# Performance work log

Measured on AMD Instinct MI355X. Metric: run time of the kernel, lower is better.

## Reference

```python
import jax, jax.numpy as jnp
import numpy as np

NEG_SLOPE = 0.2

def setup_inputs() -> dict:
    key = jax.random.key(0)
    ks = jax.random.split(key, 6)
    N, C, H, E_DIM, E = 50000, 128, 64, 16, 800000
    x = jax.random.normal(ks[0], (N, C), dtype=jnp.float32)
    edge_index = jax.random.randint(ks[1], (2, E), 0, N, dtype=jnp.int64)
    edge_attr = jax.random.normal(ks[2], (E, E_DIM), dtype=jnp.float32)
    fc_w = jax.random.normal(ks[3], (H, C), dtype=jnp.float32) * (1.0 / np.sqrt(C))
    fc_b = jnp.zeros((H,), dtype=jnp.float32)
    att_w = jax.random.normal(ks[4], (H, 2 * H + E_DIM), dtype=jnp.float32) * (1.0 / np.sqrt(2 * H + E_DIM))
    att_b = jnp.zeros((H,), dtype=jnp.float32)
    return {"x": x, "edge_index": edge_index, "edge_attr": edge_attr,
            "fc_w": fc_w, "fc_b": fc_b, "att_w": att_w, "att_b": att_b}

def reference(x, edge_index, edge_attr, fc_w, fc_b, att_w, att_b):
    # Node projection: h = fc(x), [N, H]
    h = x @ fc_w.T + fc_b
    src = edge_index[0]  # i (destination of aggregation)
    dst = edge_index[1]  # j (neighbor whose features are aggregated)
    h_i = h[src]                      # [E, H]
    h_j = h[dst]                      # [E, H]
    feat = jnp.concatenate([h_i, h_j, edge_attr], axis=-1)  # [E, 2H+edge_dim]
    alpha = jax.nn.leaky_relu(feat @ att_w.T + att_b, negative_slope=NEG_SLOPE)  # [E, H]
    # dropout is identity in eval mode (training=False)
    msg = h_j * alpha                 # [E, H]
    out = jax.ops.segment_sum(msg, src, num_segments=h.shape[0])  # scatter-add into out[i]
    return out
```

## Files before the change

kernel.cpp:

```cpp
#include <hip/hip_runtime.h>


__global__ __launch_bounds__(256) void node_kernel(
    const float* __restrict__ x,
    const float* __restrict__ fc_w, const float* __restrict__ fc_b,
    const float* __restrict__ att_w, const float* __restrict__ att_b,
    float* __restrict__ ai_out, float2* __restrict__ hjaj_out, int N)
{
    __shared__ __align__(16) float4 wF[64 * 32];
    __shared__ __align__(16) float4 wI[64 * 16];
    __shared__ __align__(16) float4 wJ[64 * 16];
    __shared__ __align__(16) float xs[4][4][128];
    __shared__ __align__(16) float hs[4][4][64];

    const int t = threadIdx.x;
    for (int idx = t; idx < 64 * 32; idx += 256) {
        int l = idx >> 5, c = idx & 31;
        wF[l * 32 + (c ^ (l & 31))] =
            *reinterpret_cast<const float4*>(fc_w + l * 128 + c * 4);
    }
    for (int idx = t; idx < 64 * 16; idx += 256) {
        int l = idx >> 4, c = idx & 15;
        wI[l * 16 + (c ^ (l & 15))] =
            *reinterpret_cast<const float4*>(att_w + l * 144 + c * 4);
        wJ[l * 16 + (c ^ (l & 15))] =
            *reinterpret_cast<const float4*>(att_w + l * 144 + 64 + c * 4);
    }
    __syncthreads();

    const int w = t >> 6, l = t & 63;
    const float bF = fc_b[l];
    const float bA = att_b[l];
    const int waveId = blockIdx.x * 4 + w;
    const int nWaves = gridDim.x * 4;
    const float2* x2 = reinterpret_cast<const float2*>(x);

    for (int n0 = waveId * 4; n0 < N; n0 += nWaves * 4) {
        const int nb = min(4, N - n0);
        #pragma unroll
        for (int m = 0; m < 4; ++m) {
            if (m < nb) {
                float2 xv = x2[(size_t)(n0 + m) * 64 + l];
                xs[w][m][2 * l] = xv.x;
                xs[w][m][2 * l + 1] = xv.y;
            }
        }
        float acc[4] = {bF, bF, bF, bF};
        #pragma unroll
        for (int c = 0; c < 32; ++c) {
            float4 wv = wF[l * 32 + (c ^ (l & 31))];
            #pragma unroll
            for (int m = 0; m < 4; ++m) {
                float4 xc = *reinterpret_cast<const float4*>(&xs[w][m][c * 4]);
                acc[m] = fmaf(wv.x, xc.x, acc[m]);
                acc[m] = fmaf(wv.y, xc.y, acc[m]);
                acc[m] = fmaf(wv.z, xc.z, acc[m]);
                acc[m] = fmaf(wv.w, xc.w, acc[m]);
            }
        }
        #pragma unroll
        for (int m = 0; m < 4; ++m) hs[w][m][l] = acc[m];
        float a2[4] = {bA, bA, bA, bA};
        float a3[4] = {0.f, 0.f, 0.f, 0.f};
        #pragma unroll
        for (int c = 0; c < 16; ++c) {
            float4 wi = wI[l * 16 + (c ^ (l & 15))];
            float4 wj = wJ[l * 16 + (c ^ (l & 15))];
            #pragma unroll
            for (int m = 0; m < 4; ++m) {
                float4 hv = *reinterpret_cast<const float4*>(&hs[w][m][c * 4]);
                a2[m] = fmaf(wi.x, hv.x, a2[m]); a2[m] = fmaf(wi.y, hv.y, a2[m]);
                a2[m] = fmaf(wi.z, hv.z, a2[m]); a2[m] = fmaf(wi.w, hv.w, a2[m]);
                a3[m] = fmaf(wj.x, hv.x, a3[m]); a3[m] = fmaf(wj.y, hv.y, a3[m]);
                a3[m] = fmaf(wj.z, hv.z, a3[m]); a3[m] = fmaf(wj.w, hv.w, a3[m]);
            }
        }
        #pragma unroll
        for (int m = 0; m < 4; ++m) {
            if (m < nb) {
                ai_out[(size_t)(n0 + m) * 64 + l] = a2[m];
                hjaj_out[(size_t)(n0 + m) * 64 + l] = make_float2(acc[m], a3[m]);
            }
        }
    }
}

__global__ __launch_bounds__(256) void edge_kernel(
    const int* __restrict__ ei,
    const float* __restrict__ ea,
    const float* __restrict__ ai,
    const float2* __restrict__ hjaj,
    const float* __restrict__ att_w,
    float* __restrict__ out, int E)
{
    __shared__ __align__(16) float4 eas[4][256];

    const int t = threadIdx.x;
    const int w = t >> 6, l = t & 63;

    float we[16];
    #pragma unroll
    for (int k = 0; k < 16; ++k) we[k] = att_w[l * 144 + 128 + k];

    const int waveId = blockIdx.x * 4 + w;
    const int nWaves = gridDim.x * 4;
    const float4* ea4 = reinterpret_cast<const float4*>(ea);
    const int fullE = E & ~63;

#define EDGE_COMPUTE(S, HD, IDX)                                               \
    {                                                                          \
        float4 v0 = eas[w][(IDX) * 4 + 0];                                     \
        float4 v1 = eas[w][(IDX) * 4 + 1];                                     \
        float4 v2 = eas[w][(IDX) * 4 + 2];                                     \
        float4 v3 = eas[w][(IDX) * 4 + 3];                                     \
        float pre = (HD).y + a_##S;                                            \
        pre = fmaf(we[0], v0.x, pre);  pre = fmaf(we[1], v0.y, pre);           \
        pre = fmaf(we[2], v0.z, pre);  pre = fmaf(we[3], v0.w, pre);           \
        pre = fmaf(we[4], v1.x, pre);  pre = fmaf(we[5], v1.y, pre);           \
        pre = fmaf(we[6], v1.z, pre);  pre = fmaf(we[7], v1.w, pre);           \
        pre = fmaf(we[8], v2.x, pre);  pre = fmaf(we[9], v2.y, pre);           \
        pre = fmaf(we[10], v2.z, pre); pre = fmaf(we[11], v2.w, pre);          \
        pre = fmaf(we[12], v3.x, pre); pre = fmaf(we[13], v3.y, pre);          \
        pre = fmaf(we[14], v3.z, pre); pre = fmaf(we[15], v3.w, pre);          \
        float alpha = pre > 0.f ? pre : 0.2f * pre;                            \
        atomicAdd(&out[(size_t)s_##S * 64 + l], (HD).x * alpha);               \
    }

    for (int e0 = waveId * 64; e0 < fullE; e0 += nWaves * 64) {
        int src = ei[e0 + l];
        int dst = ei[E + e0 + l];
        #pragma unroll
        for (int r = 0; r < 4; ++r)
            eas[w][r * 64 + l] = ea4[(size_t)e0 * 4 + r * 64 + l];
        asm volatile("s_waitcnt lgkmcnt(0)" ::: "memory");

        #pragma unroll 1
        for (int g = 0; g < 64; g += 4) {
            int s_0 = __shfl(src, g + 0), s_1 = __shfl(src, g + 1);
            int s_2 = __shfl(src, g + 2), s_3 = __shfl(src, g + 3);
            int d_0 = __shfl(dst, g + 0), d_1 = __shfl(dst, g + 1);
            int d_2 = __shfl(dst, g + 2), d_3 = __shfl(dst, g + 3);
            float a_0 = ai[(size_t)s_0 * 64 + l];
            float a_1 = ai[(size_t)s_1 * 64 + l];
            float a_2 = ai[(size_t)s_2 * 64 + l];
            float a_3 = ai[(size_t)s_3 * 64 + l];
            float2 h0 = hjaj[(size_t)d_0 * 64 + l];
            float2 h1 = hjaj[(size_t)d_1 * 64 + l];
            float2 h2 = hjaj[(size_t)d_2 * 64 + l];
            float2 h3 = hjaj[(size_t)d_3 * 64 + l];
            EDGE_COMPUTE(0, h0, g + 0);
            EDGE_COMPUTE(1, h1, g + 1);
            EDGE_COMPUTE(2, h2, g + 2);
            EDGE_COMPUTE(3, h3, g + 3);
        }
    }

    if (E > fullE && waveId == 0) {
        const int nE = E - fullE;
        int src = 0, dst = 0;
        if (l < nE) { src = ei[fullE + l]; dst = ei[E + fullE + l]; }
        #pragma unroll
        for (int r = 0; r < 4; ++r) {
            int f = r * 64 + l;
            if (f < nE * 4) eas[w][f] = ea4[(size_t)fullE * 4 + f];
        }
        asm volatile("s_waitcnt lgkmcnt(0)" ::: "memory");
        for (int e = 0; e < nE; ++e) {
            int s_0 = __shfl(src, e);
            int d_0 = __shfl(dst, e);
            float a_0 = ai[(size_t)s_0 * 64 + l];
            float2 h0 = hjaj[(size_t)d_0 * 64 + l];
            EDGE_COMPUTE(0, h0, e);
        }
    }
#undef EDGE_COMPUTE
}

extern "C" void kernel_launch(void* const* d_in, const int* in_sizes, int n_in,
                              void* d_out, int out_size, void* d_ws, size_t ws_size,
                              hipStream_t stream) {
    const float* x     = (const float*)d_in[0];
    const int*   ei    = (const int*)d_in[1];
    const float* ea    = (const float*)d_in[2];
    const float* fc_w  = (const float*)d_in[3];
    const float* fc_b  = (const float*)d_in[4];
    const float* att_w = (const float*)d_in[5];
    const float* att_b = (const float*)d_in[6];
    float* out = (float*)d_out;

    const int N = in_sizes[0] / 128;
    const int E = in_sizes[2] / 16;

    float*  ai   = (float*)d_ws;
    float2* hjaj = (float2*)((char*)d_ws + (size_t)N * 64 * sizeof(float));

    hipMemsetAsync(d_out, 0, (size_t)out_size * sizeof(float), stream);

    node_kernel<<<512, 256, 0, stream>>>(x, fc_w, fc_b, att_w, att_b, ai, hjaj, N);
    edge_kernel<<<2048, 256, 0, stream>>>(ei, ea, ai, hjaj, att_w, out, E);
}
```

Before: 266.8 us.

## Pipeline edge gathers via async global-to-LDS loads with double buffering

Restructures the edge kernel so each wave handles exactly one 64-edge tile and gathers the per-node rows (ai, h, aj) straight into LDS using global_load_lds. Loads are issued in 8-edge chunks into two alternating buffers, with explicit vmcnt waits so gathers overlap compute and atomics. The interleaved h/aj float2 layout is split into separate arrays so each gather is a 4-byte-per-lane load into LDS. The grid grows to one wave per tile with 128-thread blocks, and the hand-tuned vmcnt counts depend on exact instruction ordering, which is fragile.

```diff
diff --git a/kernel.cpp b/kernel.cpp
--- a/kernel.cpp
+++ b/kernel.cpp
@@ -1,11 +1,25 @@
 #include <hip/hip_runtime.h>
 
 
-__global__ __launch_bounds__(256) void node_kernel(
+#define GLDS4(gp, lp)                                                          \
+    __builtin_amdgcn_global_load_lds(                                          \
+        (const __attribute__((address_space(1))) unsigned int*)(gp),           \
+        (__attribute__((address_space(3))) unsigned int*)(lp), 4, 0, 0)
+#define GLDS16(gp, lp)                                                         \
+    __builtin_amdgcn_global_load_lds(                                          \
+        (const __attribute__((address_space(1))) unsigned int*)(gp),           \
+        (__attribute__((address_space(3))) unsigned int*)(lp), 16, 0, 0)
+
+#define WAITVM_(n) asm volatile("s_waitcnt vmcnt(" #n ")" ::: "memory")
+#define WAITVM(n)                                                              \
+    do { WAITVM_(n); __builtin_amdgcn_sched_barrier(0); } while (0)
+
+__global__ __launch_bounds__(256, 2) void node_kernel(
     const float* __restrict__ x,
     const float* __restrict__ fc_w, const float* __restrict__ fc_b,
     const float* __restrict__ att_w, const float* __restrict__ att_b,
-    float* __restrict__ ai_out, float2* __restrict__ hjaj_out, int N)
+    float* __restrict__ ai_out, float* __restrict__ h_out,
+    float* __restrict__ aj_out, int N)
 {
     __shared__ __align__(16) float4 wF[64 * 32];
     __shared__ __align__(16) float4 wI[64 * 16];
@@ -79,101 +93,128 @@
         for (int m = 0; m < 4; ++m) {
             if (m < nb) {
                 ai_out[(size_t)(n0 + m) * 64 + l] = a2[m];
-                hjaj_out[(size_t)(n0 + m) * 64 + l] = make_float2(acc[m], a3[m]);
+                h_out[(size_t)(n0 + m) * 64 + l]  = acc[m];
+                aj_out[(size_t)(n0 + m) * 64 + l] = a3[m];
             }
         }
     }
 }
 
-__global__ __launch_bounds__(256) void edge_kernel(
+__global__ __launch_bounds__(128) void edge_kernel(
     const int* __restrict__ ei,
     const float* __restrict__ ea,
     const float* __restrict__ ai,
-    const float2* __restrict__ hjaj,
+    const float* __restrict__ hv,
+    const float* __restrict__ aj,
     const float* __restrict__ att_w,
     float* __restrict__ out, int E)
 {
-    __shared__ __align__(16) float4 eas[4][256];
-
-    const int t = threadIdx.x;
-    const int w = t >> 6, l = t & 63;
+    __shared__ __align__(16) float lds[2][4096];
+
+    const int t = threadIdx.x, w = t >> 6, l = t & 63;
+    float* L = lds[w];
+    float* ea_s = L;
+    float* bufA = L + 1024;
+    float* bufB = L + 2560;
 
     float we[16];
     #pragma unroll
     for (int k = 0; k < 16; ++k) we[k] = att_w[l * 144 + 128 + k];
 
-    const int waveId = blockIdx.x * 4 + w;
-    const int nWaves = gridDim.x * 4;
-    const float4* ea4 = reinterpret_cast<const float4*>(ea);
-    const int fullE = E & ~63;
-
-#define EDGE_COMPUTE(S, HD, IDX)                                               \
+    const int waveId = blockIdx.x * 2 + w;
+    const int e0 = waveId * 64;
+    if (e0 >= E) return;
+    const int nE = min(64, E - e0);
+
+    int src = 0, dst = 0;
+    if (l < nE) { src = ei[e0 + l]; dst = ei[E + e0 + l]; }
+
+#define ISSUE(c, buf)                                                          \
     {                                                                          \
-        float4 v0 = eas[w][(IDX) * 4 + 0];                                     \
-        float4 v1 = eas[w][(IDX) * 4 + 1];                                     \
-        float4 v2 = eas[w][(IDX) * 4 + 2];                                     \
-        float4 v3 = eas[w][(IDX) * 4 + 3];                                     \
-        float pre = (HD).y + a_##S;                                            \
-        pre = fmaf(we[0], v0.x, pre);  pre = fmaf(we[1], v0.y, pre);           \
-        pre = fmaf(we[2], v0.z, pre);  pre = fmaf(we[3], v0.w, pre);           \
-        pre = fmaf(we[4], v1.x, pre);  pre = fmaf(we[5], v1.y, pre);           \
-        pre = fmaf(we[6], v1.z, pre);  pre = fmaf(we[7], v1.w, pre);           \
-        pre = fmaf(we[8], v2.x, pre);  pre = fmaf(we[9], v2.y, pre);           \
-        pre = fmaf(we[10], v2.z, pre); pre = fmaf(we[11], v2.w, pre);          \
-        pre = fmaf(we[12], v3.x, pre); pre = fmaf(we[13], v3.y, pre);          \
-        pre = fmaf(we[14], v3.z, pre); pre = fmaf(we[15], v3.w, pre);          \
-        float alpha = pre > 0.f ? pre : 0.2f * pre;                            \
-        atomicAdd(&out[(size_t)s_##S * 64 + l], (HD).x * alpha);               \
-    }
-
-    for (int e0 = waveId * 64; e0 < fullE; e0 += nWaves * 64) {
-        int src = ei[e0 + l];
-        int dst = ei[E + e0 + l];
+        _Pragma("unroll") for (int k = 0; k < 8; ++k) {                        \
+            int e_ = (c) * 8 + k;                                              \
+            int s_ = __shfl(src, e_);                                          \
+            int d_ = __shfl(dst, e_);                                          \
+            GLDS4(ai + (size_t)s_ * 64 + l, (buf) + k * 192);                  \
+            GLDS4(hv + (size_t)d_ * 64 + l, (buf) + k * 192 + 64);             \
+            GLDS4(aj + (size_t)d_ * 64 + l, (buf) + k * 192 + 128);            \
+        }                                                                      \
+    }
+
+#define FMA16(pre, v0, v1, v2, v3)                                             \
+    pre = fmaf(we[0], (v0).x, pre);  pre = fmaf(we[1], (v0).y, pre);           \
+    pre = fmaf(we[2], (v0).z, pre);  pre = fmaf(we[3], (v0).w, pre);           \
+    pre = fmaf(we[4], (v1).x, pre);  pre = fmaf(we[5], (v1).y, pre);           \
+    pre = fmaf(we[6], (v1).z, pre);  pre = fmaf(we[7], (v1).w, pre);           \
+    pre = fmaf(we[8], (v2).x, pre);  pre = fmaf(we[9], (v2).y, pre);           \
+    pre = fmaf(we[10], (v2).z, pre); pre = fmaf(we[11], (v2).w, pre);          \
+    pre = fmaf(we[12], (v3).x, pre); pre = fmaf(we[13], (v3).y, pre);          \
+    pre = fmaf(we[14], (v3).z, pre); pre = fmaf(we[15], (v3).w, pre)
+
+#define COMPUTE(c, buf)                                                        \
+    {                                                                          \
+        _Pragma("unroll") for (int k = 0; k < 8; ++k) {                        \
+            int e_ = (c) * 8 + k;                                              \
+            int s_ = __shfl(src, e_);                                          \
+            float av = (buf)[k * 192 + l];                                     \
+            float hh = (buf)[k * 192 + 64 + l];                                \
+            float a2 = (buf)[k * 192 + 128 + l];                               \
+            const float4* eav = reinterpret_cast<const float4*>(ea_s + e_ * 16); \
+            float4 v0 = eav[0], v1 = eav[1], v2 = eav[2], v3 = eav[3];         \
+            float pre = av + a2;                                               \
+            FMA16(pre, v0, v1, v2, v3);                                        \
+            float alpha = pre > 0.f ? pre : 0.2f * pre;                        \
+            atomicAdd(&out[(size_t)s_ * 64 + l], hh * alpha);                  \
+        }                                                                      \
+    }
+
+    if (nE == 64) {
         #pragma unroll
         for (int r = 0; r < 4; ++r)
-            eas[w][r * 64 + l] = ea4[(size_t)e0 * 4 + r * 64 + l];
-        asm volatile("s_waitcnt lgkmcnt(0)" ::: "memory");
-
-        #pragma unroll 1
-        for (int g = 0; g < 64; g += 4) {
-            int s_0 = __shfl(src, g + 0), s_1 = __shfl(src, g + 1);
-            int s_2 = __shfl(src, g + 2), s_3 = __shfl(src, g + 3);
-            int d_0 = __shfl(dst, g + 0), d_1 = __shfl(dst, g + 1);
-            int d_2 = __shfl(dst, g + 2), d_3 = __shfl(dst, g + 3);
-            float a_0 = ai[(size_t)s_0 * 64 + l];
-            float a_1 = ai[(size_t)s_1 * 64 + l];
-            float a_2 = ai[(size_t)s_2 * 64 + l];
-            float a_3 = ai[(size_t)s_3 * 64 + l];
-            float2 h0 = hjaj[(size_t)d_0 * 64 + l];
-            float2 h1 = hjaj[(size_t)d_1 * 64 + l];
-            float2 h2 = hjaj[(size_t)d_2 * 64 + l];
-            float2 h3 = hjaj[(size_t)d_3 * 64 + l];
-            EDGE_COMPUTE(0, h0, g + 0);
-            EDGE_COMPUTE(1, h1, g + 1);
-            EDGE_COMPUTE(2, h2, g + 2);
-            EDGE_COMPUTE(3, h3, g + 3);
-        }
-    }
-
-    if (E > fullE && waveId == 0) {
-        const int nE = E - fullE;
-        int src = 0, dst = 0;
-        if (l < nE) { src = ei[fullE + l]; dst = ei[E + fullE + l]; }
-        #pragma unroll
-        for (int r = 0; r < 4; ++r) {
-            int f = r * 64 + l;
-            if (f < nE * 4) eas[w][f] = ea4[(size_t)fullE * 4 + f];
-        }
-        asm volatile("s_waitcnt lgkmcnt(0)" ::: "memory");
+            GLDS16(ea + (size_t)e0 * 16 + r * 256 + l * 4, ea_s + r * 256);
+
+        ISSUE(0, bufA);
+        ISSUE(1, bufB);
+        WAITVM(24);
+        COMPUTE(0, bufA);
+        ISSUE(2, bufA);
+        WAITVM(32);
+        COMPUTE(1, bufB);
+        ISSUE(3, bufB);
+        WAITVM(32);
+        COMPUTE(2, bufA);
+        ISSUE(4, bufA);
+        WAITVM(32);
+        COMPUTE(3, bufB);
+        ISSUE(5, bufB);
+        WAITVM(32);
+        COMPUTE(4, bufA);
+        ISSUE(6, bufA);
+        WAITVM(32);
+        COMPUTE(5, bufB);
+        ISSUE(7, bufB);
+        WAITVM(32);
+        COMPUTE(6, bufA);
+        WAITVM(8);
+        COMPUTE(7, bufB);
+    } else {
         for (int e = 0; e < nE; ++e) {
-            int s_0 = __shfl(src, e);
-            int d_0 = __shfl(dst, e);
-            float a_0 = ai[(size_t)s_0 * 64 + l];
-            float2 h0 = hjaj[(size_t)d_0 * 64 + l];
-            EDGE_COMPUTE(0, h0, e);
-        }
-    }
-#undef EDGE_COMPUTE
+            int s_ = __shfl(src, e);
+            int d_ = __shfl(dst, e);
+            float av = ai[(size_t)s_ * 64 + l];
+            float hh = hv[(size_t)d_ * 64 + l];
+            float a2 = aj[(size_t)d_ * 64 + l];
+            const float4* eav = reinterpret_cast<const float4*>(ea + ((size_t)e0 + e) * 16);
+            float4 v0 = eav[0], v1 = eav[1], v2 = eav[2], v3 = eav[3];
+            float pre = av + a2;
+            FMA16(pre, v0, v1, v2, v3);
+            float alpha = pre > 0.f ? pre : 0.2f * pre;
+            atomicAdd(&out[(size_t)s_ * 64 + l], hh * alpha);
+        }
+    }
+#undef ISSUE
+#undef COMPUTE
+#undef FMA16
 }
 
 extern "C" void kernel_launch(void* const* d_in, const int* in_sizes, int n_in,
@@ -191,11 +232,15 @@
     const int N = in_sizes[0] / 128;
     const int E = in_sizes[2] / 16;
 
-    float*  ai   = (float*)d_ws;
-    float2* hjaj = (float2*)((char*)d_ws + (size_t)N * 64 * sizeof(float));
+    float* ai = (float*)d_ws;
+    float* hv = ai + (size_t)N * 64;
+    float* aj = hv + (size_t)N * 64;
 
     hipMemsetAsync(d_out, 0, (size_t)out_size * sizeof(float), stream);
 
-    node_kernel<<<512, 256, 0, stream>>>(x, fc_w, fc_b, att_w, att_b, ai, hjaj, N);
-    edge_kernel<<<2048, 256, 0, stream>>>(ei, ea, ai, hjaj, att_w, out, E);
+    node_kernel<<<512, 256, 0, stream>>>(x, fc_w, fc_b, att_w, att_b, ai, hv, aj, N);
+
+    const int tiles = (E + 63) / 64;
+    const int eblocks = (tiles + 1) / 2;
+    edge_kernel<<<eblocks, 128, 0, stream>>>(ei, ea, ai, hv, aj, att_w, out, E);
 }
```

Result: slower. 509.4 us (+90.9%).
